# Performance work log

Measured on AMD Instinct MI355X. Metric: run time of the kernel, lower is better.

The kernel has to match this reference:

```python
import jax, jax.numpy as jnp
import numpy as np

FULL_SCALE = 128
TOPK = 3
R = 0.5


def setup_inputs() -> dict:
    key = jax.random.key(0)
    k1, k2, k3, k4 = jax.random.split(key, 4)
    B, Na, Nb, D = 8, 4096, 4096, 64
    a_coords = jax.random.randint(k1, (B, Na, 3), 0, FULL_SCALE * 16, dtype=jnp.int32)
    b_coords = jax.random.randint(k2, (B, Nb, 3), 0, FULL_SCALE * 16, dtype=jnp.int32)
    a_feats = jax.random.normal(k3, (B, Na, D), dtype=jnp.float32)
    b_feats = jax.random.normal(k4, (B, Nb, D), dtype=jnp.float32)
    return {"a_feats": a_feats, "b_feats": b_feats,
            "a_coords": a_coords, "b_coords": b_coords}


def reference(a_feats, b_feats, a_coords, b_coords):
    # coords are divided by 16 (integer floor div) before the distance computation
    ca = (a_coords // 16).astype(jnp.float32)  # [B, Na, 3]
    cb = (b_coords // 16).astype(jnp.float32)  # [B, Nb, 3]

    # pairwise euclidean distance per batch group (torch.cdist equivalent)
    d2 = (jnp.sum(ca * ca, -1, keepdims=True)
          + jnp.sum(cb * cb, -1)[:, None, :]
          - 2.0 * jnp.einsum('bnd,bmd->bnm', ca, cb))  # [B, Na, Nb]
    dist = jnp.sqrt(jnp.clip(d2, 0.0, None)) / FULL_SCALE

    # top-k nearest neighbors (argsort ascending, take first TOPK)
    neg_top, idx = jax.lax.top_k(-dist, TOPK)  # idx: [B, Na, K]
    dist_w = R - jnp.clip(-neg_top, 0.0, R)    # [B, Na, K]

    # gather neighbor features: [B, Na, K, D]
    B = b_feats.shape[0]
    gathered = b_feats[jnp.arange(B)[:, None, None], idx]
    tmp = jnp.einsum('bnkd,bnk->bnd', gathered, dist_w)  # weighted sum over K

    # ME.cat(a, tmp): concatenate features along channel dim
    return jnp.concatenate([a_feats, tmp], axis=-1)  # [B, Na, 2D]
```

## Files before the change

kernel.cpp:

```cpp
#include <hip/hip_runtime.h>


#define NA 4096
#define NB 4096
#define FD 64
#define WPB 8
#define MPW 4
#define BLOCK (WPB * 64)
#define APB (WPB * MPW)
#define NBPAD 4352
#define PADG 0x7FF00000

static __device__ __forceinline__ int med3_i32(int a, int b, int c) {
    int d;
    asm("v_med3_i32 %0, %1, %2, %3" : "=v"(d) : "v"(a), "v"(b), "v"(c));
    return d;
}

static __device__ __forceinline__ int mad_i24(int a, int b, int c) {
    int d;
    asm("v_mad_i32_i24 %0, %1, %2, %3" : "=v"(d) : "v"(a), "v"(b), "v"(c));
    return d;
}

__global__ __launch_bounds__(BLOCK, 8) void knn_gather_kernel(
    const float* __restrict__ a_feats,
    const float* __restrict__ b_feats,
    const int*   __restrict__ a_coords,
    const int*   __restrict__ b_coords,
    float* __restrict__ out)
{
    __shared__ __align__(16) unsigned s_pb[NBPAD];
    __shared__ __align__(16) int      s_G[NBPAD];
    __shared__ int s_xs[129];
    __shared__ int s_hist[128];
    __shared__ int s_cur[128];

    const int batch = blockIdx.y;
    const int tid   = threadIdx.x;

    if (tid < 128) s_hist[tid] = 0;
    if (tid < 256) { s_pb[NB + tid] = 0u; s_G[NB + tid] = PADG; }
    __syncthreads();

    const int* bc = b_coords + (size_t)batch * NB * 3;
    int pbv[8];
#pragma unroll
    for (int k = 0; k < 8; ++k) {
        const int i = tid + (k << 9);
        const int x = bc[3 * i + 0] >> 4;
        const int y = bc[3 * i + 1] >> 4;
        const int z = bc[3 * i + 2] >> 4;
        pbv[k] = x | (y << 8) | (z << 16);
        atomicAdd(&s_hist[x], 1);
    }
    __syncthreads();

    if (tid < 128) s_xs[tid + 1] = s_hist[tid];
    if (tid == 0)  s_xs[0] = 0;
    __syncthreads();
    for (int d = 1; d < 128; d <<= 1) {
        int v = 0;
        if (tid < 128) {
            v = s_xs[tid + 1];
            if (tid >= d) v += s_xs[tid + 1 - d];
        }
        __syncthreads();
        if (tid < 128) s_xs[tid + 1] = v;
        __syncthreads();
    }
    if (tid < 128) s_cur[tid] = s_xs[tid];
    __syncthreads();

#pragma unroll
    for (int k = 0; k < 8; ++k) {
        const int pb  = pbv[k];
        const int x   = pb & 0xFF;
        const int y   = (pb >> 8)  & 0xFF;
        const int z   = (pb >> 16) & 0xFF;
        const int pos = atomicAdd(&s_cur[x], 1);
        s_pb[pos] = (unsigned)pb;
        s_G[pos]  = ((__mul24(x, x) + __mul24(y, y) + __mul24(z, z)) << 12)
                    | (tid + (k << 9));
    }
    __syncthreads();

    const int wave  = tid >> 6;
    const int lane  = tid & 63;
    const int nbase = blockIdx.x * APB + wave * MPW;

    const int* ac = a_coords + ((size_t)batch * NA + nbase) * 3;
    int pa0, pa1, pa2, pa3;
    {
        const int x0 = ac[0] >> 4, y0 = ac[1]  >> 4, z0 = ac[2]  >> 4;
        const int x1 = ac[3] >> 4, y1 = ac[4]  >> 4, z1 = ac[5]  >> 4;
        const int x2 = ac[6] >> 4, y2 = ac[7]  >> 4, z2 = ac[8]  >> 4;
        const int x3 = ac[9] >> 4, y3 = ac[10] >> 4, z3 = ac[11] >> 4;
        pa0 = x0 | (y0 << 8) | (z0 << 16);
        pa1 = x1 | (y1 << 8) | (z1 << 16);
        pa2 = x2 | (y2 << 8) | (z2 << 16);
        pa3 = x3 | (y3 << 8) | (z3 << 16);
    }
    const int neg8k = -8192;

    int k0_0 = 0x7FFFFFFF, k1_0 = 0x7FFFFFFF, k2_0 = 0x7FFFFFFF;
    int k0_1 = 0x7FFFFFFF, k1_1 = 0x7FFFFFFF, k2_1 = 0x7FFFFFFF;
    int k0_2 = 0x7FFFFFFF, k1_2 = 0x7FFFFFFF, k2_2 = 0x7FFFFFFF;
    int k0_3 = 0x7FFFFFFF, k1_3 = 0x7FFFFFFF, k2_3 = 0x7FFFFFFF;

    const uint4* pb4 = (const uint4*)s_pb;
    const int4*  G4  = (const int4*)s_G;
    uint4 P = pb4[lane];
    int4  G = G4[lane];

#define KNN_ONE(PJ, GJ)                                              \
    {                                                                \
        const int Pj = (int)(PJ);                                    \
        const int Gj = (GJ);                                         \
        {   const int t   = __builtin_amdgcn_sdot4(pa0, Pj, 0, false); \
            const int key = mad_i24(t, neg8k, Gj);                   \
            const int n0 = min(k0_0, key);                           \
            const int n1 = med3_i32(k0_0, k1_0, key);                \
            const int n2 = med3_i32(k1_0, k2_0, key);                \
            k0_0 = n0; k1_0 = n1; k2_0 = n2; }                       \
        {   const int t   = __builtin_amdgcn_sdot4(pa1, Pj, 0, false); \
            const int key = mad_i24(t, neg8k, Gj);                   \
            const int n0 = min(k0_1, key);                           \
            const int n1 = med3_i32(k0_1, k1_1, key);                \
            const int n2 = med3_i32(k1_1, k2_1, key);                \
            k0_1 = n0; k1_1 = n1; k2_1 = n2; }                       \
        {   const int t   = __builtin_amdgcn_sdot4(pa2, Pj, 0, false); \
            const int key = mad_i24(t, neg8k, Gj);                   \
            const int n0 = min(k0_2, key);                           \
            const int n1 = med3_i32(k0_2, k1_2, key);                \
            const int n2 = med3_i32(k1_2, k2_2, key);                \
            k0_2 = n0; k1_2 = n1; k2_2 = n2; }                       \
        {   const int t   = __builtin_amdgcn_sdot4(pa3, Pj, 0, false); \
            const int key = mad_i24(t, neg8k, Gj);                   \
            const int n0 = min(k0_3, key);                           \
            const int n1 = med3_i32(k0_3, k1_3, key);                \
            const int n2 = med3_i32(k1_3, k2_3, key);                \
            k0_3 = n0; k1_3 = n1; k2_3 = n2; }                       \
    }

#pragma unroll 2
    for (int k = 0; k < 16; ++k) {
        const int qn = lane + ((k + 1) << 6);
        const uint4 Pn = pb4[qn];
        const int4  Gn = G4[qn];

        KNN_ONE(P.x, G.x)
        KNN_ONE(P.y, G.y)
        KNN_ONE(P.z, G.z)
        KNN_ONE(P.w, G.w)

        P = Pn; G = Gn;
    }
#undef KNN_ONE

    const float* bfb = b_feats + (size_t)batch * NB * FD;
    int K0[MPW] = {k0_0, k0_1, k0_2, k0_3};
    int K1[MPW] = {k1_0, k1_1, k1_2, k1_3};
    int K2[MPW] = {k2_0, k2_1, k2_2, k2_3};
    const int PA[MPW] = {pa0, pa1, pa2, pa3};

#pragma unroll
    for (int m = 0; m < MPW; ++m) {
        int a0 = K0[m], a1 = K1[m], a2 = K2[m];
#pragma unroll
        for (int d = 1; d < 64; d <<= 1) {
            const int b0 = __shfl_xor(a0, d, 64);
            const int b1 = __shfl_xor(a1, d, 64);
            const int b2 = __shfl_xor(a2, d, 64);
            const int h0 = max(a0, b0);
            const int l1 = min(a1, b1);
            const int c2 = min(a2, b2);
            a0 = min(a0, b0);
            a1 = min(h0, l1);
            a2 = med3_i32(c2, l1, h0);
        }
        const int aa = __builtin_amdgcn_sdot4(PA[m], PA[m], 0, false);
        const int i0 = a0 & 4095, i1 = a1 & 4095, i2 = a2 & 4095;
        const float d0 = sqrtf((float)((a0 >> 12) + aa)) * (1.0f / 128.0f);
        const float d1 = sqrtf((float)((a1 >> 12) + aa)) * (1.0f / 128.0f);
        const float d2 = sqrtf((float)((a2 >> 12) + aa)) * (1.0f / 128.0f);
        const float w0 = 0.5f - fminf(d0, 0.5f);
        const float w1 = 0.5f - fminf(d1, 0.5f);
        const float w2 = 0.5f - fminf(d2, 0.5f);

        const size_t row = (size_t)batch * NA + (nbase + m);
        const float g = w0 * bfb[i0 * FD + lane]
                      + w1 * bfb[i1 * FD + lane]
                      + w2 * bfb[i2 * FD + lane];
        out[row * 128 + lane]      = a_feats[row * FD + lane];
        out[row * 128 + 64 + lane] = g;
    }
}

extern "C" void kernel_launch(void* const* d_in, const int* in_sizes, int n_in,
                              void* d_out, int out_size, void* d_ws, size_t ws_size,
                              hipStream_t stream) {
    const float* a_feats  = (const float*)d_in[0];
    const float* b_feats  = (const float*)d_in[1];
    const int*   a_coords = (const int*)d_in[2];
    const int*   b_coords = (const int*)d_in[3];
    float* out = (float*)d_out;

    const int B = in_sizes[0] / (NA * FD);
    dim3 grid(NA / APB, B);
    knn_gather_kernel<<<grid, BLOCK, 0, stream>>>(a_feats, b_feats, a_coords,
                                                  b_coords, out);
}
```

Before: 104.7 us.

## Sort query points by x and scan only an x-window of sorted candidates

Each block ranks its 32 query points by x coordinate, so every wave gets four nearby points. The wave then scans only the x-sorted candidate chunks within ±16 cells of its x-range instead of all 4096 candidates. If any third-nearest squared distance exceeds 288, the window could have missed a closer point, so the wave falls back to the full scan. This cuts most of the distance and top-k work, in exchange for extra rank-sort and verification overhead, possible wave divergence on fallback, and scattered output row writes.

```diff
diff --git a/kernel.cpp b/kernel.cpp
--- a/kernel.cpp
+++ b/kernel.cpp
@@ -10,6 +10,8 @@
 #define APB (WPB * MPW)
 #define NBPAD 4352
 #define PADG 0x7FF00000
+#define WIN 16
+#define THRD2 288
 
 static __device__ __forceinline__ int med3_i32(int a, int b, int c) {
     int d;
@@ -35,12 +37,19 @@
     __shared__ int s_xs[129];
     __shared__ int s_hist[128];
     __shared__ int s_cur[128];
-
-    const int batch = blockIdx.y;
-    const int tid   = threadIdx.x;
+    __shared__ int s_akey[APB];
+    __shared__ int s_ord[APB];
+
+    const int batch  = blockIdx.y;
+    const int tid    = threadIdx.x;
+    const int nbase0 = blockIdx.x * APB;
 
     if (tid < 128) s_hist[tid] = 0;
     if (tid < 256) { s_pb[NB + tid] = 0u; s_G[NB + tid] = PADG; }
+    if (tid < APB) {
+        const int ax = a_coords[((size_t)batch * NA + nbase0 + tid) * 3] >> 4;
+        s_akey[tid] = (ax << 8) | tid;
+    }
     __syncthreads();
 
     const int* bc = b_coords + (size_t)batch * NB * 3;
@@ -55,6 +64,14 @@
         atomicAdd(&s_hist[x], 1);
     }
     __syncthreads();
+
+    if (tid < APB) {
+        const int my = s_akey[tid];
+        int r = 0;
+#pragma unroll
+        for (int j = 0; j < APB; ++j) r += (s_akey[j] < my) ? 1 : 0;
+        s_ord[r] = tid;
+    }
 
     if (tid < 128) s_xs[tid + 1] = s_hist[tid];
     if (tid == 0)  s_xs[0] = 0;
@@ -85,17 +102,22 @@
     }
     __syncthreads();
 
-    const int wave  = tid >> 6;
-    const int lane  = tid & 63;
-    const int nbase = blockIdx.x * APB + wave * MPW;
-
-    const int* ac = a_coords + ((size_t)batch * NA + nbase) * 3;
+    const int wave = tid >> 6;
+    const int lane = tid & 63;
+    const int si0 = s_ord[wave * MPW + 0];
+    const int si1 = s_ord[wave * MPW + 1];
+    const int si2 = s_ord[wave * MPW + 2];
+    const int si3 = s_ord[wave * MPW + 3];
+
+    const int* acb = a_coords + (size_t)batch * NA * 3;
     int pa0, pa1, pa2, pa3;
     {
-        const int x0 = ac[0] >> 4, y0 = ac[1]  >> 4, z0 = ac[2]  >> 4;
-        const int x1 = ac[3] >> 4, y1 = ac[4]  >> 4, z1 = ac[5]  >> 4;
-        const int x2 = ac[6] >> 4, y2 = ac[7]  >> 4, z2 = ac[8]  >> 4;
-        const int x3 = ac[9] >> 4, y3 = ac[10] >> 4, z3 = ac[11] >> 4;
+        const int r0 = (nbase0 + si0) * 3, r1 = (nbase0 + si1) * 3;
+        const int r2 = (nbase0 + si2) * 3, r3 = (nbase0 + si3) * 3;
+        const int x0 = acb[r0] >> 4, y0 = acb[r0+1] >> 4, z0 = acb[r0+2] >> 4;
+        const int x1 = acb[r1] >> 4, y1 = acb[r1+1] >> 4, z1 = acb[r1+2] >> 4;
+        const int x2 = acb[r2] >> 4, y2 = acb[r2+1] >> 4, z2 = acb[r2+2] >> 4;
+        const int x3 = acb[r3] >> 4, y3 = acb[r3+1] >> 4, z3 = acb[r3+2] >> 4;
         pa0 = x0 | (y0 << 8) | (z0 << 16);
         pa1 = x1 | (y1 << 8) | (z1 << 16);
         pa2 = x2 | (y2 << 8) | (z2 << 16);
@@ -103,6 +125,20 @@
     }
     const int neg8k = -8192;
 
+    int klo, khi;
+    {
+        const int ax0 = pa0 & 0xFF, ax1 = pa1 & 0xFF;
+        const int ax2 = pa2 & 0xFF, ax3 = pa3 & 0xFF;
+        const int xmn = min(min(ax0, ax1), min(ax2, ax3));
+        const int xmx = max(max(ax0, ax1), max(ax2, ax3));
+        int blo = xmn - WIN;     blo = blo < 0   ? 0   : blo;
+        int bhi = xmx + WIN + 1; bhi = bhi > 128 ? 128 : bhi;
+        const int lo = s_xs[blo];
+        const int hi = s_xs[bhi];
+        klo = lo >> 8;
+        khi = (hi + 255) >> 8;
+    }
+
     int k0_0 = 0x7FFFFFFF, k1_0 = 0x7FFFFFFF, k2_0 = 0x7FFFFFFF;
     int k0_1 = 0x7FFFFFFF, k1_1 = 0x7FFFFFFF, k2_1 = 0x7FFFFFFF;
     int k0_2 = 0x7FFFFFFF, k1_2 = 0x7FFFFFFF, k2_2 = 0x7FFFFFFF;
@@ -110,8 +146,8 @@
 
     const uint4* pb4 = (const uint4*)s_pb;
     const int4*  G4  = (const int4*)s_G;
-    uint4 P = pb4[lane];
-    int4  G = G4[lane];
+    uint4 P = pb4[lane + (klo << 6)];
+    int4  G = G4[lane + (klo << 6)];
 
 #define KNN_ONE(PJ, GJ)                                              \
     {                                                                \
@@ -143,8 +179,32 @@
             k0_3 = n0; k1_3 = n1; k2_3 = n2; }                       \
     }
 
+#define MERGE_ALL()                                                  \
+    {                                                                \
+        int K0[MPW] = {k0_0, k0_1, k0_2, k0_3};                      \
+        int K1[MPW] = {k1_0, k1_1, k1_2, k1_3};                      \
+        int K2[MPW] = {k2_0, k2_1, k2_2, k2_3};                      \
+        _Pragma("unroll")                                            \
+        for (int m = 0; m < MPW; ++m) {                              \
+            int a0 = K0[m], a1 = K1[m], a2 = K2[m];                  \
+            _Pragma("unroll")                                        \
+            for (int d = 1; d < 64; d <<= 1) {                       \
+                const int b0 = __shfl_xor(a0, d, 64);                \
+                const int b1 = __shfl_xor(a1, d, 64);                \
+                const int b2 = __shfl_xor(a2, d, 64);                \
+                const int h0 = max(a0, b0);                          \
+                const int l1 = min(a1, b1);                          \
+                const int c2 = min(a2, b2);                          \
+                a0 = min(a0, b0);                                    \
+                a1 = min(h0, l1);                                    \
+                a2 = med3_i32(c2, l1, h0);                           \
+            }                                                        \
+            A0[m] = a0; A1[m] = a1; A2[m] = a2;                      \
+        }                                                            \
+    }
+
 #pragma unroll 2
-    for (int k = 0; k < 16; ++k) {
+    for (int k = klo; k < khi; ++k) {
         const int qn = lane + ((k + 1) << 6);
         const uint4 Pn = pb4[qn];
         const int4  Gn = G4[qn];
@@ -156,30 +216,50 @@
 
         P = Pn; G = Gn;
     }
+
+    const int PA[MPW] = {pa0, pa1, pa2, pa3};
+    int AA[MPW];
+#pragma unroll
+    for (int m = 0; m < MPW; ++m)
+        AA[m] = __builtin_amdgcn_sdot4(PA[m], PA[m], 0, false);
+
+    int A0[MPW], A1[MPW], A2[MPW];
+    MERGE_ALL()
+
+    bool bad = false;
+#pragma unroll
+    for (int m = 0; m < MPW; ++m)
+        bad = bad | ((unsigned)((A2[m] >> 12) + AA[m]) > (unsigned)THRD2);
+    if (__any(bad)) {
+        k0_0 = 0x7FFFFFFF; k1_0 = 0x7FFFFFFF; k2_0 = 0x7FFFFFFF;
+        k0_1 = 0x7FFFFFFF; k1_1 = 0x7FFFFFFF; k2_1 = 0x7FFFFFFF;
+        k0_2 = 0x7FFFFFFF; k1_2 = 0x7FFFFFFF; k2_2 = 0x7FFFFFFF;
+        k0_3 = 0x7FFFFFFF; k1_3 = 0x7FFFFFFF; k2_3 = 0x7FFFFFFF;
+        P = pb4[lane];
+        G = G4[lane];
+#pragma unroll 2
+        for (int k = 0; k < 16; ++k) {
+            const int qn = lane + ((k + 1) << 6);
+            const uint4 Pn = pb4[qn];
+            const int4  Gn = G4[qn];
+            KNN_ONE(P.x, G.x)
+            KNN_ONE(P.y, G.y)
+            KNN_ONE(P.z, G.z)
+            KNN_ONE(P.w, G.w)
+            P = Pn; G = Gn;
+        }
+        MERGE_ALL()
+    }
 #undef KNN_ONE
+#undef MERGE_ALL
 
     const float* bfb = b_feats + (size_t)batch * NB * FD;
-    int K0[MPW] = {k0_0, k0_1, k0_2, k0_3};
-    int K1[MPW] = {k1_0, k1_1, k1_2, k1_3};
-    int K2[MPW] = {k2_0, k2_1, k2_2, k2_3};
-    const int PA[MPW] = {pa0, pa1, pa2, pa3};
+    const int SI[MPW] = {si0, si1, si2, si3};
 
 #pragma unroll
     for (int m = 0; m < MPW; ++m) {
-        int a0 = K0[m], a1 = K1[m], a2 = K2[m];
-#pragma unroll
-        for (int d = 1; d < 64; d <<= 1) {
-            const int b0 = __shfl_xor(a0, d, 64);
-            const int b1 = __shfl_xor(a1, d, 64);
-            const int b2 = __shfl_xor(a2, d, 64);
-            const int h0 = max(a0, b0);
-            const int l1 = min(a1, b1);
-            const int c2 = min(a2, b2);
-            a0 = min(a0, b0);
-            a1 = min(h0, l1);
-            a2 = med3_i32(c2, l1, h0);
-        }
-        const int aa = __builtin_amdgcn_sdot4(PA[m], PA[m], 0, false);
+        const int a0 = A0[m], a1 = A1[m], a2 = A2[m];
+        const int aa = AA[m];
         const int i0 = a0 & 4095, i1 = a1 & 4095, i2 = a2 & 4095;
         const float d0 = sqrtf((float)((a0 >> 12) + aa)) * (1.0f / 128.0f);
         const float d1 = sqrtf((float)((a1 >> 12) + aa)) * (1.0f / 128.0f);
@@ -188,7 +268,7 @@
         const float w1 = 0.5f - fminf(d1, 0.5f);
         const float w2 = 0.5f - fminf(d2, 0.5f);
 
-        const size_t row = (size_t)batch * NA + (nbase + m);
+        const size_t row = (size_t)batch * NA + (nbase0 + SI[m]);
         const float g = w0 * bfb[i0 * FD + lane]
                       + w1 * bfb[i1 * FD + lane]
                       + w2 * bfb[i2 * FD + lane];
```

New measurement: 94.69 us. 1.11x faster.
